# Kernel optimization log

Hardware: AMD Instinct MI355X
Metric: run time of the kernel (lower is better)

Reference implementation:

```python
import jax, jax.numpy as jnp
import numpy as np

K = 3          # kernel size
K2 = K * K     # ope_channels


def setup_inputs() -> dict:
    key = jax.random.key(0)
    k1, k2, k3, k4, k5 = jax.random.split(key, 5)
    b, c, h, w = 8, 64, 128, 128
    out_c = 64
    x = jax.random.normal(k1, (b, c, h, w), dtype=jnp.float32)
    # conv weight: (in_channels, out_channels, k, k) as in the torch module
    weight = jax.random.normal(k2, (c, out_c, K, K), dtype=jnp.float32) * 0.05
    bias = jax.random.normal(k3, (out_c,), dtype=jnp.float32) * 0.05
    # operator MLP: Linear(K2 -> K2*K2); torch weight layout (out_features, in_features)
    op_w = jax.random.normal(k4, (K2 * K2, K2), dtype=jnp.float32) * 0.1
    op_b = jax.random.normal(k5, (K2 * K2,), dtype=jnp.float32) * 0.01
    return {"x": x, "weight": weight, "bias": bias, "op_w": op_w, "op_b": op_b}


def _unfold(x):
    # F.unfold(kernel=3, stride=1, pad=1) -> patches ordered (c, ki, kj)
    b, c, h, w = x.shape
    xp = jnp.pad(x, ((0, 0), (0, 0), (1, 1), (1, 1)))
    # (b, c, K2, h, w) with K2 ordered row-major over (ki, kj), matching torch
    patches = jnp.stack([xp[:, :, i:i + h, j:j + w]
                         for i in range(K) for j in range(K)], axis=2)
    return patches.transpose(0, 1, 3, 4, 2)  # (b, c, h, w, K2)


def reference(x, weight, bias, op_w, op_b):
    b, c, h, w = x.shape
    xu = _unfold(x)  # (b, c, h, w, K2)
    # per-pixel patch norm over channels -> (b, h, w, K2)
    n = jnp.sqrt(jnp.sum(xu * xu, axis=1))
    # per-pixel dynamic operator: (b, h, w, K2, K2)
    op = jnp.tanh(n @ op_w.T + op_b).reshape(b, h, w, K2, K2)
    # apply operator: bchw j , bhw jk -> bchw k
    x_op = jnp.einsum('bchwj,bhwjk->bchwk', xu, op)
    # final conv weight contraction: weight (in, out, K, K) -> (out, in, K2)
    wr = weight.reshape(c, -1, K2).transpose(1, 0, 2)
    out = jnp.einsum('bchwk,ock->bohw', x_op + xu, wr)
    return out + bias[None, :, None, None]
```

## Files before the change

### kernel.cpp

```cpp
#include <hip/hip_runtime.h>
#include <math.h>
#include <stdint.h>

#define HW   128
#define CIN  64
#define OC   64
#define TW   16
#define TH   4
#define HLW  18
#define HLH  6
#define HLN  (HLW*HLH)
#define SXR  109
#define NPX  (TW*TH)
#define K2   9
#define KTOT (CIN*K2)
#define ZROW 584

typedef __bf16 bf16x8 __attribute__((ext_vector_type(8)));
typedef float  f32x4  __attribute__((ext_vector_type(4)));

__device__ __forceinline__ ushort f32_to_bf16_rne(float f) {
    union { float f; uint32_t u; } x; x.f = f;
    return (ushort)((x.u + 0x7FFF + ((x.u >> 16) & 1)) >> 16);
}
__device__ __forceinline__ float bf16u_to_f32(ushort u) {
    union { uint32_t u; float f; } x; x.u = ((uint32_t)u) << 16;
    return x.f;
}

__global__ void prep_weight(const float* __restrict__ w, ushort* __restrict__ wt) {
    int n = blockIdx.x * 256 + threadIdx.x;
    int o = n / KTOT;
    int r = n - o * KTOT;
    int kt = r >> 6;
    int c  = r & 63;
    wt[n] = f32_to_bf16_rne(w[(c * OC + o) * K2 + kt]);
}

__global__ __launch_bounds__(256, 2)
void dyf_main(const float* __restrict__ x,
              const float* __restrict__ bias,
              const float* __restrict__ op_w,
              const float* __restrict__ op_b,
              const ushort* __restrict__ wt,
              float* __restrict__ out)
{
    __shared__ float  sx[CIN * SXR];
    __shared__ float  sT[HLN];
    __shared__ ushort sop[NPX * 82];
    __shared__ ushort zt[32 * ZROW];

    const int tid  = threadIdx.x;
    const int lane = tid & 63;
    const int wv   = tid >> 6;
    const int b    = blockIdx.z;
    const int h0   = blockIdx.y * TH;
    const int w0   = blockIdx.x * TW;

    bf16x8 areg[18];
    {
        const ushort* ap = wt + (wv * 16 + (lane & 15)) * KTOT + ((lane >> 4) * 8);
        #pragma unroll
        for (int s = 0; s < 18; ++s)
            areg[s] = *reinterpret_cast<const bf16x8*>(ap + s * 32);
    }

    const float* __restrict__ xb = x + (size_t)b * CIN * HW * HW;
    #pragma unroll
    for (int it = 0; it < 27; ++it) {
        int i  = tid + it * 256;
        int c  = i / HLN;
        int r  = i - c * HLN;
        int hy = r / HLW;
        int hx = r - hy * HLW;
        int gy = h0 - 1 + hy;
        int gx = w0 - 1 + hx;
        float v = 0.f;
        if ((unsigned)gy < HW && (unsigned)gx < HW)
            v = xb[c * HW * HW + gy * HW + gx];
        sx[c * SXR + r] = v;
    }
    __syncthreads();

    if (tid < HLN) {
        float s = 0.f;
        #pragma unroll 16
        for (int c = 0; c < CIN; ++c) { float v = sx[c * SXR + tid]; s += v * v; }
        sT[tid] = s;
    }
    __syncthreads();

    {
        const int px  = tid >> 2;
        const int q   = tid & 3;
        const int py  = px >> 4, pxx = px & 15;
        float nrm[9];
        #pragma unroll
        for (int j = 0; j < 9; ++j)
            nrm[j] = sqrtf(sT[(py + j / 3) * HLW + pxx + (j % 3)]);
        const int m0   = q * 20;
        const int mcnt = (q == 3) ? 21 : 20;
        for (int mm = 0; mm < mcnt; ++mm) {
            int m = m0 + mm;
            float a = op_b[m];
            #pragma unroll
            for (int j = 0; j < 9; ++j) a += nrm[j] * op_w[m * 9 + j];
            sop[px * 82 + m] = f32_to_bf16_rne(tanhf(a));
        }
    }
    __syncthreads();

    #pragma unroll 1
    for (int hh = 0; hh < 2; ++hh) {
        {
            const int pxl = tid >> 3;
            const int px  = hh * 32 + pxl;
            const int cq  = tid & 7;
            const int py  = px >> 4, pxx = px & 15;

            float xu[8][9];
            #pragma unroll
            for (int cc = 0; cc < 8; ++cc) {
                const int base = (cq * 8 + cc) * SXR;
                #pragma unroll
                for (int j = 0; j < 9; ++j)
                    xu[cc][j] = sx[base + (py + j / 3) * HLW + pxx + (j % 3)];
            }
            #pragma unroll
            for (int k = 0; k < 9; ++k) {
                float opj[9];
                #pragma unroll
                for (int j = 0; j < 9; ++j)
                    opj[j] = bf16u_to_f32(sop[px * 82 + j * 9 + k]);
                float y[8];
                #pragma unroll
                for (int cc = 0; cc < 8; ++cc) {
                    float s = xu[cc][k];
                    #pragma unroll
                    for (int j = 0; j < 9; ++j) s += xu[cc][j] * opj[j];
                    y[cc] = s;
                }
                uint32_t p0, p1, p2, p3;
                asm("v_cvt_pk_bf16_f32 %0, %1, %2" : "=v"(p0) : "v"(y[0]), "v"(y[1]));
                asm("v_cvt_pk_bf16_f32 %0, %1, %2" : "=v"(p1) : "v"(y[2]), "v"(y[3]));
                asm("v_cvt_pk_bf16_f32 %0, %1, %2" : "=v"(p2) : "v"(y[4]), "v"(y[5]));
                asm("v_cvt_pk_bf16_f32 %0, %1, %2" : "=v"(p3) : "v"(y[6]), "v"(y[7]));
                *reinterpret_cast<uint4*>(&zt[pxl * ZROW + k * 64 + cq * 8])
                    = make_uint4(p0, p1, p2, p3);
            }
        }
        __syncthreads();

        {
            f32x4 acc[2];
            acc[0] = f32x4{0.f, 0.f, 0.f, 0.f};
            acc[1] = f32x4{0.f, 0.f, 0.f, 0.f};
            const int bl = lane & 15;
            const int g8 = (lane >> 4) * 8;
            #pragma unroll
            for (int s = 0; s < 18; ++s) {
                #pragma unroll
                for (int nf = 0; nf < 2; ++nf) {
                    const ushort* bp = &zt[(nf * 16 + bl) * ZROW + s * 32 + g8];
                    bf16x8 bfr = *reinterpret_cast<const bf16x8*>(bp);
                    acc[nf] = __builtin_amdgcn_mfma_f32_16x16x32_bf16(areg[s], bfr, acc[nf], 0, 0, 0);
                }
            }
            #pragma unroll
            for (int nf = 0; nf < 2; ++nf) {
                const int py = hh * 2 + nf;
                #pragma unroll
                for (int i = 0; i < 4; ++i) {
                    const int o = wv * 16 + (lane >> 4) * 4 + i;
                    out[(((size_t)b * OC + o) * HW + (h0 + py)) * HW + w0 + bl]
                        = acc[nf][i] + bias[o];
                }
            }
        }
        __syncthreads();
    }
}

extern "C" void kernel_launch(void* const* d_in, const int* in_sizes, int n_in,
                              void* d_out, int out_size, void* d_ws, size_t ws_size,
                              hipStream_t stream) {
    const float* x      = (const float*)d_in[0];
    const float* weight = (const float*)d_in[1];
    const float* bias   = (const float*)d_in[2];
    const float* op_w   = (const float*)d_in[3];
    const float* op_b   = (const float*)d_in[4];
    float*  out = (float*)d_out;
    ushort* wt  = (ushort*)d_ws;

    prep_weight<<<dim3((OC * KTOT) / 256), dim3(256), 0, stream>>>(weight, wt);

    dim3 grid(HW / TW, HW / TH, 8);
    dyf_main<<<grid, dim3(256), 0, stream>>>(x, bias, op_w, op_b, wt, out);
}
```

Baseline: 200.1 us.

## Build MFMA B operands in registers per wave and fold identity into operator

Each wave now owns one pixel row. It builds the transformed patch operand directly in registers as packed bf16 MFMA B fragments, so the zt shared staging buffer and the two-half loop with its barriers are gone. The wave computes all 64 output channels by streaming A fragments from global weights instead of keeping 18 preloaded A registers. The operator is stored in fp32 with the identity term (+1 on the diagonal) folded in, which removes the separate residual add. In exchange each thread holds 81 operator floats plus 18 packed vectors, raising register pressure, and it repeats global or L2 weight loads inside the MFMA loop.

```diff
diff --git a/kernel.cpp b/kernel.cpp
--- a/kernel.cpp
+++ b/kernel.cpp
@@ -11,22 +11,21 @@
 #define HLH  6
 #define HLN  (HLW*HLH)
 #define SXR  109
-#define NPX  (TW*TH)
 #define K2   9
 #define KTOT (CIN*K2)
-#define ZROW 584
+#define SOPR 81
 
-typedef __bf16 bf16x8 __attribute__((ext_vector_type(8)));
-typedef float  f32x4  __attribute__((ext_vector_type(4)));
+typedef __bf16  bf16x8 __attribute__((ext_vector_type(8)));
+typedef float   f32x4  __attribute__((ext_vector_type(4)));
+typedef uint32_t u32x4 __attribute__((ext_vector_type(4)));
 
 __device__ __forceinline__ ushort f32_to_bf16_rne(float f) {
     union { float f; uint32_t u; } x; x.f = f;
     return (ushort)((x.u + 0x7FFF + ((x.u >> 16) & 1)) >> 16);
 }
-__device__ __forceinline__ float bf16u_to_f32(ushort u) {
-    union { uint32_t u; float f; } x; x.u = ((uint32_t)u) << 16;
-    return x.f;
-}
+
+#define PKBF16(dst, lo, hi) \
+    asm("v_cvt_pk_bf16_f32 %0, %1, %2" : "=v"(dst) : "v"(lo), "v"(hi))
 
 __global__ void prep_weight(const float* __restrict__ w, ushort* __restrict__ wt) {
     int n = blockIdx.x * 256 + threadIdx.x;
@@ -45,10 +44,9 @@
               const ushort* __restrict__ wt,
               float* __restrict__ out)
 {
-    __shared__ float  sx[CIN * SXR];
-    __shared__ float  sT[HLN];
-    __shared__ ushort sop[NPX * 82];
-    __shared__ ushort zt[32 * ZROW];
+    __shared__ float sx[CIN * SXR];
+    __shared__ float sT[HLN];
+    __shared__ float sop[64 * SOPR];
 
     const int tid  = threadIdx.x;
     const int lane = tid & 63;
@@ -57,28 +55,22 @@
     const int h0   = blockIdx.y * TH;
     const int w0   = blockIdx.x * TW;
 
-    bf16x8 areg[18];
     {
-        const ushort* ap = wt + (wv * 16 + (lane & 15)) * KTOT + ((lane >> 4) * 8);
+        const float* __restrict__ xb = x + (size_t)b * CIN * HW * HW;
         #pragma unroll
-        for (int s = 0; s < 18; ++s)
-            areg[s] = *reinterpret_cast<const bf16x8*>(ap + s * 32);
-    }
-
-    const float* __restrict__ xb = x + (size_t)b * CIN * HW * HW;
-    #pragma unroll
-    for (int it = 0; it < 27; ++it) {
-        int i  = tid + it * 256;
-        int c  = i / HLN;
-        int r  = i - c * HLN;
-        int hy = r / HLW;
-        int hx = r - hy * HLW;
-        int gy = h0 - 1 + hy;
-        int gx = w0 - 1 + hx;
-        float v = 0.f;
-        if ((unsigned)gy < HW && (unsigned)gx < HW)
-            v = xb[c * HW * HW + gy * HW + gx];
-        sx[c * SXR + r] = v;
+        for (int it = 0; it < 27; ++it) {
+            int i  = tid + it * 256;
+            int c  = i / HLN;
+            int r  = i - c * HLN;
+            int hy = r / HLW;
+            int hx = r - hy * HLW;
+            int gy = h0 - 1 + hy;
+            int gx = w0 - 1 + hx;
+            float v = 0.f;
+            if ((unsigned)gy < HW && (unsigned)gx < HW)
+                v = xb[c * HW * HW + gy * HW + gx];
+            sx[c * SXR + r] = v;
+        }
     }
     __syncthreads();
 
@@ -91,93 +83,96 @@
     __syncthreads();
 
     {
-        const int px  = tid >> 2;
-        const int q   = tid & 3;
-        const int py  = px >> 4, pxx = px & 15;
+        const int px = tid >> 2;
+        const int q  = tid & 3;
+        const int py = px >> 4, pxx = px & 15;
         float nrm[9];
         #pragma unroll
         for (int j = 0; j < 9; ++j)
             nrm[j] = sqrtf(sT[(py + j / 3) * HLW + pxx + (j % 3)]);
-        const int m0   = q * 20;
-        const int mcnt = (q == 3) ? 21 : 20;
-        for (int mm = 0; mm < mcnt; ++mm) {
-            int m = m0 + mm;
-            float a = op_b[m];
+        const int nkt = (q == 0) ? 3 : 2;
+        for (int t = 0; t < 3; ++t) {
+            if (t >= nkt) break;
+            const int kt = (q == 0) ? ((t == 2) ? 8 : t) : (q * 2 + t);
             #pragma unroll
-            for (int j = 0; j < 9; ++j) a += nrm[j] * op_w[m * 9 + j];
-            sop[px * 82 + m] = f32_to_bf16_rne(tanhf(a));
+            for (int j = 0; j < 9; ++j) {
+                const int m = j * 9 + kt;
+                float a = op_b[m];
+                #pragma unroll
+                for (int jj = 0; jj < 9; ++jj) a += nrm[jj] * op_w[m * 9 + jj];
+                float v = tanhf(a);
+                if (j == kt) v += 1.0f;
+                sop[px * SOPR + m] = v;
+            }
         }
     }
     __syncthreads();
 
-    #pragma unroll 1
-    for (int hh = 0; hh < 2; ++hh) {
-        {
-            const int pxl = tid >> 3;
-            const int px  = hh * 32 + pxl;
-            const int cq  = tid & 7;
-            const int py  = px >> 4, pxx = px & 15;
+    const int pxx = lane & 15;
+    const int g   = lane >> 4;
+    const int py  = wv;
 
-            float xu[8][9];
+    float opf[81];
+    {
+        const float* srcp = &sop[(wv * 16 + pxx) * SOPR];
+        #pragma unroll
+        for (int m = 0; m < 81; ++m) opf[m] = srcp[m];
+    }
+
+    u32x4 zw[18];
+    #pragma unroll
+    for (int chalf = 0; chalf < 2; ++chalf) {
+        #pragma unroll
+        for (int t = 0; t < 4; ++t) {
+            const int c0 = chalf * 32 + g * 8 + 2 * t;
+            float xu0[9], xu1[9];
             #pragma unroll
-            for (int cc = 0; cc < 8; ++cc) {
-                const int base = (cq * 8 + cc) * SXR;
-                #pragma unroll
-                for (int j = 0; j < 9; ++j)
-                    xu[cc][j] = sx[base + (py + j / 3) * HLW + pxx + (j % 3)];
+            for (int j = 0; j < 9; ++j) {
+                const int pos = (py + j / 3) * HLW + pxx + (j % 3);
+                xu0[j] = sx[c0 * SXR + pos];
+                xu1[j] = sx[(c0 + 1) * SXR + pos];
             }
             #pragma unroll
-            for (int k = 0; k < 9; ++k) {
-                float opj[9];
+            for (int kt = 0; kt < 9; ++kt) {
+                float y0 = 0.f, y1 = 0.f;
                 #pragma unroll
-                for (int j = 0; j < 9; ++j)
-                    opj[j] = bf16u_to_f32(sop[px * 82 + j * 9 + k]);
-                float y[8];
-                #pragma unroll
-                for (int cc = 0; cc < 8; ++cc) {
-                    float s = xu[cc][k];
-                    #pragma unroll
-                    for (int j = 0; j < 9; ++j) s += xu[cc][j] * opj[j];
-                    y[cc] = s;
+                for (int j = 0; j < 9; ++j) {
+                    y0 += xu0[j] * opf[j * 9 + kt];
+                    y1 += xu1[j] * opf[j * 9 + kt];
                 }
-                uint32_t p0, p1, p2, p3;
-                asm("v_cvt_pk_bf16_f32 %0, %1, %2" : "=v"(p0) : "v"(y[0]), "v"(y[1]));
-                asm("v_cvt_pk_bf16_f32 %0, %1, %2" : "=v"(p1) : "v"(y[2]), "v"(y[3]));
-                asm("v_cvt_pk_bf16_f32 %0, %1, %2" : "=v"(p2) : "v"(y[4]), "v"(y[5]));
-                asm("v_cvt_pk_bf16_f32 %0, %1, %2" : "=v"(p3) : "v"(y[6]), "v"(y[7]));
-                *reinterpret_cast<uint4*>(&zt[pxl * ZROW + k * 64 + cq * 8])
-                    = make_uint4(p0, p1, p2, p3);
+                uint32_t pk;
+                PKBF16(pk, y0, y1);
+                zw[2 * kt + chalf][t] = pk;
             }
         }
-        __syncthreads();
+    }
 
-        {
-            f32x4 acc[2];
-            acc[0] = f32x4{0.f, 0.f, 0.f, 0.f};
-            acc[1] = f32x4{0.f, 0.f, 0.f, 0.f};
-            const int bl = lane & 15;
-            const int g8 = (lane >> 4) * 8;
+    __builtin_amdgcn_sched_barrier(0);
+
+    {
+        f32x4 acc[4];
+        #pragma unroll
+        for (int mr = 0; mr < 4; ++mr) acc[mr] = f32x4{0.f, 0.f, 0.f, 0.f};
+
+        #pragma unroll
+        for (int s = 0; s < 18; ++s) {
+            const bf16x8 bfr = __builtin_bit_cast(bf16x8, zw[s]);
             #pragma unroll
-            for (int s = 0; s < 18; ++s) {
-                #pragma unroll
-                for (int nf = 0; nf < 2; ++nf) {
-                    const ushort* bp = &zt[(nf * 16 + bl) * ZROW + s * 32 + g8];
-                    bf16x8 bfr = *reinterpret_cast<const bf16x8*>(bp);
-                    acc[nf] = __builtin_amdgcn_mfma_f32_16x16x32_bf16(areg[s], bfr, acc[nf], 0, 0, 0);
-                }
-            }
-            #pragma unroll
-            for (int nf = 0; nf < 2; ++nf) {
-                const int py = hh * 2 + nf;
-                #pragma unroll
-                for (int i = 0; i < 4; ++i) {
-                    const int o = wv * 16 + (lane >> 4) * 4 + i;
-                    out[(((size_t)b * OC + o) * HW + (h0 + py)) * HW + w0 + bl]
-                        = acc[nf][i] + bias[o];
-                }
+            for (int mr = 0; mr < 4; ++mr) {
+                const bf16x8 af = *reinterpret_cast<const bf16x8*>(
+                    wt + (mr * 16 + pxx) * KTOT + s * 32 + g * 8);
+                acc[mr] = __builtin_amdgcn_mfma_f32_16x16x32_bf16(af, bfr, acc[mr], 0, 0, 0);
             }
         }
-        __syncthreads();
+        #pragma unroll
+        for (int mr = 0; mr < 4; ++mr) {
+            #pragma unroll
+            for (int ii = 0; ii < 4; ++ii) {
+                const int o = mr * 16 + g * 4 + ii;
+                out[(((size_t)b * OC + o) * HW + (h0 + wv)) * HW + w0 + pxx]
+                    = acc[mr][ii] + bias[o];
+            }
+        }
     }
 }
 
```

New measurement: 217.5 us. +8.7%, slower.
